# Kernel optimization log

Hardware: AMD Instinct MI355X
Metric: run time of the kernel (lower is better)

Reference implementation:

```python
import jax, jax.numpy as jnp
import numpy as np

B, LATENT = 8192, 1024
NR, NC = 12, 12                      # nb_rows, nb_cols
H0, W0 = NR + 2, NC + 2              # 14x14 after reshape
EPS = 1e-5
SLOPE = 0.01                         # LeakyReLU default


def setup_inputs() -> dict:
    key = jax.random.key(0)
    ks = jax.random.split(key, 9)
    s = 0.05
    return {
        "x": jax.random.normal(ks[0], (B, LATENT), jnp.float32),
        "fc_w": jax.random.normal(ks[1], (H0 * W0 * 36, LATENT), jnp.float32) * s,
        "fc_b": jax.random.normal(ks[2], (H0 * W0 * 36,), jnp.float32) * s,
        "conv_w": jax.random.normal(ks[3], (16, 36, 2, 2), jnp.float32) * s,
        "conv_b": jax.random.normal(ks[4], (16,), jnp.float32) * s,
        "gamma": jnp.ones((16,), jnp.float32),
        "beta": jnp.zeros((16,), jnp.float32),
        # locally-connected weights: (out_ch, in_ch, Hout, Wout, k*k)
        "lw1": jax.random.normal(ks[5], (6, 16, H0 - 1, W0 - 1, 4), jnp.float32) * s,
        "lw2": jax.random.normal(ks[6], (1, 6, H0 - 2, W0 - 2, 4), jnp.float32) * s,
    }


def _leaky(x):
    return jnp.where(x >= 0, x, SLOPE * x)


def _local_conv2(x, w):
    # x: (B,C,H,W); w: (O,C,Ho,Wo,4) with k=2, stride 1, no padding
    Ho, Wo = w.shape[2], w.shape[3]
    patches = jnp.stack(
        [x[:, :, dy:dy + Ho, dx:dx + Wo] for dy in (0, 1) for dx in (0, 1)],
        axis=-1)  # (B,C,Ho,Wo,4)
    return jnp.einsum('bchwk,ochwk->bohw', patches, w)


def reference(x, fc_w, fc_b, conv_w, conv_b, gamma, beta, lw1, lw2):
    # fc -> view(B, H0, W0, 36) -> permute to NCHW
    h = x @ fc_w.T + fc_b
    h = h.reshape(B, H0, W0, 36).transpose(0, 3, 1, 2)  # (B,36,14,14)
    # Conv2d k=2 padding='same' (torch pads bottom/right for even kernels)
    h = jax.lax.conv_general_dilated(
        h, conv_w, window_strides=(1, 1), padding=((0, 1), (0, 1)),
        dimension_numbers=('NCHW', 'OIHW', 'NCHW')) + conv_b[None, :, None, None]
    h = _leaky(h)
    # BatchNorm2d (training mode: batch stats, biased var)
    mu = h.mean(axis=(0, 2, 3), keepdims=True)
    var = h.var(axis=(0, 2, 3), keepdims=True)
    h = (h - mu) * jax.lax.rsqrt(var + EPS)
    h = h * gamma[None, :, None, None] + beta[None, :, None, None]
    # locally-connected stack: 14x14 -> 13x13 -> 12x12
    h = _leaky(_local_conv2(h, lw1))
    return _local_conv2(h, lw2)  # (B,1,12,12)
```

## Files before the change

kernel.cpp:

```cpp
#include <hip/hip_runtime.h>


#define SLOPE 0.01f

typedef __bf16 bf16x8 __attribute__((ext_vector_type(8)));
typedef float f32x4 __attribute__((ext_vector_type(4)));

typedef const __attribute__((address_space(1))) void* gas_ptr;
typedef __attribute__((address_space(3))) void* las_ptr;

__device__ __forceinline__ void load16_to_lds(const void* g, void* l) {
  __builtin_amdgcn_global_load_lds((gas_ptr)g, (las_ptr)l, 16, 0, 0);
}

__device__ __forceinline__ unsigned short f2bf(float f) {
  union { float f; unsigned int u; } v; v.f = f;
  unsigned int r = v.u + 0x7FFFu + ((v.u >> 16) & 1u);
  return (unsigned short)(r >> 16);
}
__device__ __forceinline__ float bfbits2f(unsigned int bits16) {
  union { unsigned int u; float f; } v; v.u = bits16 << 16;
  return v.f;
}
__device__ __forceinline__ float leaky(float v) { return v >= 0.f ? v : SLOPE * v; }

__global__ void k_cast_x(const float* __restrict__ x, unsigned short* __restrict__ xb,
                         float* __restrict__ stats) {
  if (blockIdx.x == 0 && threadIdx.x < 32) stats[threadIdx.x] = 0.f;
  int gid = blockIdx.x * 256 + threadIdx.x;
  const float4* x4 = (const float4*)x;
  float4 a = x4[gid * 2], b = x4[gid * 2 + 1];
  union { unsigned short s[8]; uint4 v; } o;
  o.s[0] = f2bf(a.x); o.s[1] = f2bf(a.y); o.s[2] = f2bf(a.z); o.s[3] = f2bf(a.w);
  o.s[4] = f2bf(b.x); o.s[5] = f2bf(b.y); o.s[6] = f2bf(b.z); o.s[7] = f2bf(b.w);
  ((uint4*)xb)[gid] = o.v;
}

__global__ void k_fold(const float* __restrict__ fc_w, const float* __restrict__ fc_b,
                       const float* __restrict__ conv_w, const float* __restrict__ conv_b,
                       unsigned short* __restrict__ Wc, float* __restrict__ bc) {
  __shared__ float cw[2304];
  int blk = blockIdx.x, og = blockIdx.y, t = threadIdx.x;
  if (blk == 196) {
    if (og != 0) return;
    uint4 z = make_uint4(0, 0, 0, 0);
    uint4* dst = (uint4*)(Wc + 3136 * 1024);
    for (int i = t; i < 8192; i += 256) dst[i] = z;
    for (int i = 3136 + t; i < 3200; i += 256) bc[i] = 0.f;
    return;
  }
  for (int i = t; i < 2304; i += 256) cw[i] = conv_w[i];
  __syncthreads();
  int i0 = blk / 14, j0 = blk - (blk / 14) * 14;
  float acc[4][4];
#pragma unroll
  for (int o = 0; o < 4; o++)
#pragma unroll
    for (int q = 0; q < 4; q++) acc[o][q] = 0.f;
  for (int c = 0; c < 36; c++) {
#pragma unroll
    for (int dy = 0; dy < 2; dy++) {
      int ii = i0 + dy; if (ii > 13) continue;
#pragma unroll
      for (int dx = 0; dx < 2; dx++) {
        int jj = j0 + dx; if (jj > 13) continue;
        int row = (ii * 14 + jj) * 36 + c;
        float4 f = *(const float4*)(fc_w + row * 1024 + t * 4);
        int kk = dy * 2 + dx;
#pragma unroll
        for (int oo = 0; oo < 4; oo++) {
          int o = og * 4 + oo;
          float w = cw[(o * 36 + c) * 4 + kk];
          acc[oo][0] += w * f.x; acc[oo][1] += w * f.y;
          acc[oo][2] += w * f.z; acc[oo][3] += w * f.w;
        }
      }
    }
  }
#pragma unroll
  for (int oo = 0; oo < 4; oo++) {
    int o = og * 4 + oo;
    int n = o * 196 + i0 * 14 + j0;
    union { unsigned short s[4]; uint2 v; } u;
    u.s[0] = f2bf(acc[oo][0]); u.s[1] = f2bf(acc[oo][1]);
    u.s[2] = f2bf(acc[oo][2]); u.s[3] = f2bf(acc[oo][3]);
    *(uint2*)(Wc + n * 1024 + t * 4) = u.v;
  }
  if (og == 0 && t < 16) {
    int o = t;
    float b = conv_b[o];
    for (int c = 0; c < 36; c++)
      for (int dy = 0; dy < 2; dy++) {
        int ii = i0 + dy; if (ii > 13) continue;
        for (int dx = 0; dx < 2; dx++) {
          int jj = j0 + dx; if (jj > 13) continue;
          b += cw[(o * 36 + c) * 4 + dy * 2 + dx] * fc_b[(ii * 14 + jj) * 36 + c];
        }
      }
    bc[o * 196 + i0 * 14 + j0] = b;
  }
}

__global__ __launch_bounds__(256, 4) void k_gemm(const unsigned short* __restrict__ Xb,
                                                 const unsigned short* __restrict__ Wcb,
                                                 const float* __restrict__ bc,
                                                 unsigned short* __restrict__ h2,
                                                 float* __restrict__ stats) {
  __shared__ __align__(16) char lds[32768];
  __shared__ float red[4][4];
  const int t = threadIdx.x;
  const int w = t >> 6, lane = t & 63;
  const int quad = lane >> 4, l15 = lane & 15;
  const int m0 = blockIdx.y * 128, n0 = blockIdx.x * 128;
  const int mrow = t & 127, tko = t >> 7;
  const unsigned short* ga = Xb + (m0 + mrow) * 1024 + tko * 8;
  const unsigned short* gb = Wcb + (n0 + mrow) * 1024 + tko * 8;
  const int wbase = w * 1024;
  const int wm0 = (w >> 1) * 64, wn0 = (w & 1) * 64;

  f32x4 acc[4][4];
#pragma unroll
  for (int a = 0; a < 4; a++)
#pragma unroll
    for (int b = 0; b < 4; b++) acc[a][b] = (f32x4){0.f, 0.f, 0.f, 0.f};

  auto stage = [&](int buf, int kb) {
    char* sA = lds + buf * 16384;
    char* sB = sA + 8192;
    load16_to_lds(ga + kb,      sA + wbase);
    load16_to_lds(ga + kb + 16, sA + 4096 + wbase);
    load16_to_lds(gb + kb,      sB + wbase);
    load16_to_lds(gb + kb + 16, sB + 4096 + wbase);
  };
  auto compute = [&](int buf) {
    char* lA = lds + buf * 16384;
    char* lB = lA + 8192;
    bf16x8 af[4], bfr[4];
#pragma unroll
    for (int mb = 0; mb < 4; mb++)
      af[mb] = *(const bf16x8*)(lA + quad * 2048 + (wm0 + mb * 16 + l15) * 16);
#pragma unroll
    for (int nb = 0; nb < 4; nb++)
      bfr[nb] = *(const bf16x8*)(lB + quad * 2048 + (wn0 + nb * 16 + l15) * 16);
#pragma unroll
    for (int mb = 0; mb < 4; mb++)
#pragma unroll
      for (int nb = 0; nb < 4; nb++)
        acc[mb][nb] = __builtin_amdgcn_mfma_f32_16x16x32_bf16(af[mb], bfr[nb], acc[mb][nb], 0, 0, 0);
  };

  stage(0, 0);
  __syncthreads();
  int cur = 0;
  for (int kb = 0; kb < 992; kb += 32) {
    stage(cur ^ 1, kb + 32);
    compute(cur);
    __syncthreads();
    cur ^= 1;
  }
  compute(cur);

  const int cLo = n0 / 196;
  const int cHi = (n0 + 127) / 196;
  float ss0 = 0.f, ss1 = 0.f, sq0 = 0.f, sq1 = 0.f;
#pragma unroll
  for (int nb = 0; nb < 4; nb++) {
    int col = n0 + wn0 + nb * 16 + l15;
    float bias = bc[col];
    int ch = col / 196;
    bool hi = (ch != cLo);
    bool valid = col < 3136;
    float cs = 0.f, cq = 0.f;
#pragma unroll
    for (int mb = 0; mb < 4; mb++) {
#pragma unroll
      for (int r = 0; r < 4; r++) {
        int row = m0 + wm0 + mb * 16 + quad * 4 + r;
        float v = leaky(acc[mb][nb][r] + bias);
        h2[row * 3200 + col] = f2bf(v);
        cs += v; cq += v * v;
      }
    }
    if (valid) {
      if (hi) { ss1 += cs; sq1 += cq; } else { ss0 += cs; sq0 += cq; }
    }
  }
#pragma unroll
  for (int off = 1; off < 64; off <<= 1) {
    ss0 += __shfl_xor(ss0, off, 64);
    ss1 += __shfl_xor(ss1, off, 64);
    sq0 += __shfl_xor(sq0, off, 64);
    sq1 += __shfl_xor(sq1, off, 64);
  }
  if (lane == 0) { red[w][0] = ss0; red[w][1] = ss1; red[w][2] = sq0; red[w][3] = sq1; }
  __syncthreads();
  if (t == 0) {
    float a0 = red[0][0] + red[1][0] + red[2][0] + red[3][0];
    float a1 = red[0][1] + red[1][1] + red[2][1] + red[3][1];
    float b0 = red[0][2] + red[1][2] + red[2][2] + red[3][2];
    float b1 = red[0][3] + red[1][3] + red[2][3] + red[3][3];
    atomicAdd(&stats[cLo], a0);
    atomicAdd(&stats[16 + cLo], b0);
    if (cHi != cLo && cHi < 16) {
      atomicAdd(&stats[cHi], a1);
      atomicAdd(&stats[16 + cHi], b1);
    }
  }
}

__global__ __launch_bounds__(256) void k_tail(const unsigned short* __restrict__ h2,
                                              const float* __restrict__ stats,
                                              const float* __restrict__ gamma,
                                              const float* __restrict__ beta,
                                              const float* __restrict__ lw1,
                                              const float* __restrict__ lw2,
                                              float* __restrict__ out) {
  __shared__ unsigned short h3[4 * 3138];
  __shared__ float h4[4 * 1015];
  __shared__ float sc[16], sh[16];
  int b0 = blockIdx.x * 4, t = threadIdx.x;
  if (t < 16) {
    const float inv = 1.f / 1605632.f;
    float mean = stats[t] * inv;
    float var = stats[16 + t] * inv - mean * mean;
    float rstd = rsqrtf(var + 1e-5f);
    float s = gamma[t] * rstd;
    sc[t] = s; sh[t] = beta[t] - mean * s;
  }
  __syncthreads();
  for (int i = t; i < 6272; i += 256) {
    int bb = i / 1568, q = i - bb * 1568;
    int n = q * 2, o = n / 196;
    unsigned int u = *(const unsigned int*)(h2 + (b0 + bb) * 3200 + n);
    float v0 = bfbits2f(u & 0xffffu) * sc[o] + sh[o];
    float v1 = bfbits2f(u >> 16) * sc[o] + sh[o];
    unsigned int pk = (unsigned int)f2bf(v0) | ((unsigned int)f2bf(v1) << 16);
    *(unsigned int*)(h3 + bb * 3138 + n) = pk;
  }
  __syncthreads();
  for (int u = t; u < 312; u += 256) {
    int bb = u & 3, rest = u >> 2;
    int o = rest / 13, y = rest - o * 13;
    float acc[13];
#pragma unroll
    for (int x = 0; x < 13; x++) acc[x] = 0.f;
    const unsigned short* hb = h3 + bb * 3138;
    for (int c = 0; c < 16; c++) {
      float r0[14], r1[14];
      const unsigned int* p0 = (const unsigned int*)(hb + c * 196 + y * 14);
      const unsigned int* p1 = (const unsigned int*)(hb + c * 196 + (y + 1) * 14);
#pragma unroll
      for (int q = 0; q < 7; q++) {
        unsigned int v0 = p0[q], v1 = p1[q];
        r0[2 * q] = bfbits2f(v0 & 0xffffu); r0[2 * q + 1] = bfbits2f(v0 >> 16);
        r1[2 * q] = bfbits2f(v1 & 0xffffu); r1[2 * q + 1] = bfbits2f(v1 >> 16);
      }
      const float4* wp4 = (const float4*)(lw1 + (((o * 16 + c) * 13 + y) * 13) * 4);
#pragma unroll
      for (int x = 0; x < 13; x++) {
        float4 wv = wp4[x];
        acc[x] += r0[x] * wv.x + r0[x + 1] * wv.y +
                  r1[x] * wv.z + r1[x + 1] * wv.w;
      }
    }
#pragma unroll
    for (int x = 0; x < 13; x++)
      h4[bb * 1015 + (o * 13 + y) * 13 + x] = leaky(acc[x]);
  }
  __syncthreads();
  for (int oi = t; oi < 576; oi += 256) {
    int pos = oi >> 2, bb = oi & 3;
    int y = pos / 12, x = pos - y * 12;
    float a = 0.f;
    const float* hp = h4 + bb * 1015;
    const float4* w4 = (const float4*)lw2;
#pragma unroll
    for (int c = 0; c < 6; c++) {
      float4 wv = w4[(c * 12 + y) * 12 + x];
      int hb = c * 169 + y * 13 + x;
      a += hp[hb] * wv.x + hp[hb + 1] * wv.y +
           hp[hb + 13] * wv.z + hp[hb + 14] * wv.w;
    }
    out[(b0 + bb) * 144 + pos] = a;
  }
}

extern "C" void kernel_launch(void* const* d_in, const int* in_sizes, int n_in,
                              void* d_out, int out_size, void* d_ws, size_t ws_size,
                              hipStream_t stream) {
  const float* x      = (const float*)d_in[0];
  const float* fc_w   = (const float*)d_in[1];
  const float* fc_b   = (const float*)d_in[2];
  const float* conv_w = (const float*)d_in[3];
  const float* conv_b = (const float*)d_in[4];
  const float* gamma  = (const float*)d_in[5];
  const float* beta   = (const float*)d_in[6];
  const float* lw1    = (const float*)d_in[7];
  const float* lw2    = (const float*)d_in[8];

  char* ws = (char*)d_ws;
  unsigned short* Xb    = (unsigned short*)(ws);
  unsigned short* Wc    = (unsigned short*)(ws + 16777216);
  float*          bc    = (float*)(ws + 23330816);
  float*          stats = (float*)(ws + 23343616);
  unsigned short* h2    = (unsigned short*)(ws + 23343744);

  k_cast_x<<<4096, 256, 0, stream>>>(x, Xb, stats);
  k_fold<<<dim3(197, 4), 256, 0, stream>>>(fc_w, fc_b, conv_w, conv_b, Wc, bc);
  k_gemm<<<dim3(25, 64), 256, 0, stream>>>(Xb, Wc, bc, h2, stats);
  k_tail<<<2048, 256, 0, stream>>>(h2, stats, gamma, beta, lw1, lw2, (float*)d_out);
}
```

Baseline: 384.9 us.

## Use 256x256 GEMM tiles with 512 threads and XCD-aware block mapping

The fused fc+conv GEMM moves from 128x128 tiles with 256 threads to 256x256 tiles with 512 threads (8 waves, each 128x64). A 1-D grid is remapped so consecutive M blocks share an XCD for L2 reuse. The padded N is extended to 3328 with zeroed weights/bias. The double-buffered LDS pipeline is replaced by a single buffer with two barriers per k-step, which loses load/compute overlap. Stats atomics are computed per wave.

```diff
diff --git a/kernel.cpp b/kernel.cpp
--- a/kernel.cpp
+++ b/kernel.cpp
@@ -45,8 +45,8 @@
     if (og != 0) return;
     uint4 z = make_uint4(0, 0, 0, 0);
     uint4* dst = (uint4*)(Wc + 3136 * 1024);
-    for (int i = t; i < 8192; i += 256) dst[i] = z;
-    for (int i = 3136 + t; i < 3200; i += 256) bc[i] = 0.f;
+    for (int i = t; i < 24576; i += 256) dst[i] = z;
+    for (int i = 3136 + t; i < 3328; i += 256) bc[i] = 0.f;
     return;
   }
   for (int i = t; i < 2304; i += 256) cw[i] = conv_w[i];
@@ -101,87 +101,79 @@
   }
 }
 
-__global__ __launch_bounds__(256, 4) void k_gemm(const unsigned short* __restrict__ Xb,
+__global__ __launch_bounds__(512, 1) void k_gemm(const unsigned short* __restrict__ Xb,
                                                  const unsigned short* __restrict__ Wcb,
                                                  const float* __restrict__ bc,
                                                  unsigned short* __restrict__ h2,
                                                  float* __restrict__ stats) {
   __shared__ __align__(16) char lds[32768];
-  __shared__ float red[4][4];
+  __shared__ float red[8][4];
   const int t = threadIdx.x;
   const int w = t >> 6, lane = t & 63;
   const int quad = lane >> 4, l15 = lane & 15;
-  const int m0 = blockIdx.y * 128, n0 = blockIdx.x * 128;
-  const int mrow = t & 127, tko = t >> 7;
+  const int d = blockIdx.x;
+  const int xcd = d & 7, j = d >> 3;
+  const int mblk = xcd * 4 + (j & 3);
+  const int nblk = j >> 2;
+  const int m0 = mblk * 256, n0 = nblk * 256;
+  const int mrow = t & 255, tko = t >> 8;
   const unsigned short* ga = Xb + (m0 + mrow) * 1024 + tko * 8;
   const unsigned short* gb = Wcb + (n0 + mrow) * 1024 + tko * 8;
-  const int wbase = w * 1024;
-  const int wm0 = (w >> 1) * 64, wn0 = (w & 1) * 64;
-
-  f32x4 acc[4][4];
-#pragma unroll
-  for (int a = 0; a < 4; a++)
+  char* lA = lds;
+  char* lB = lds + 16384;
+  const int wm = w >> 2, wn = w & 3;
+  const int wm0 = wm * 128, wn0 = wn * 64;
+
+  f32x4 acc[8][4];
+#pragma unroll
+  for (int a = 0; a < 8; a++)
 #pragma unroll
     for (int b = 0; b < 4; b++) acc[a][b] = (f32x4){0.f, 0.f, 0.f, 0.f};
 
-  auto stage = [&](int buf, int kb) {
-    char* sA = lds + buf * 16384;
-    char* sB = sA + 8192;
-    load16_to_lds(ga + kb,      sA + wbase);
-    load16_to_lds(ga + kb + 16, sA + 4096 + wbase);
-    load16_to_lds(gb + kb,      sB + wbase);
-    load16_to_lds(gb + kb + 16, sB + 4096 + wbase);
-  };
-  auto compute = [&](int buf) {
-    char* lA = lds + buf * 16384;
-    char* lB = lA + 8192;
-    bf16x8 af[4], bfr[4];
-#pragma unroll
-    for (int mb = 0; mb < 4; mb++)
-      af[mb] = *(const bf16x8*)(lA + quad * 2048 + (wm0 + mb * 16 + l15) * 16);
+  for (int kb = 0; kb < 1024; kb += 32) {
+    __syncthreads();
+    load16_to_lds(ga + kb,      lA + t * 16);
+    load16_to_lds(ga + kb + 16, lA + 8192 + t * 16);
+    load16_to_lds(gb + kb,      lB + t * 16);
+    load16_to_lds(gb + kb + 16, lB + 8192 + t * 16);
+    __syncthreads();
+
+    bf16x8 af[8], bfr[4];
+#pragma unroll
+    for (int mb = 0; mb < 8; mb++)
+      af[mb] = *(const bf16x8*)(lA + quad * 4096 + (wm0 + mb * 16 + l15) * 16);
 #pragma unroll
     for (int nb = 0; nb < 4; nb++)
-      bfr[nb] = *(const bf16x8*)(lB + quad * 2048 + (wn0 + nb * 16 + l15) * 16);
-#pragma unroll
-    for (int mb = 0; mb < 4; mb++)
+      bfr[nb] = *(const bf16x8*)(lB + quad * 4096 + (wn0 + nb * 16 + l15) * 16);
+#pragma unroll
+    for (int mb = 0; mb < 8; mb++)
 #pragma unroll
       for (int nb = 0; nb < 4; nb++)
         acc[mb][nb] = __builtin_amdgcn_mfma_f32_16x16x32_bf16(af[mb], bfr[nb], acc[mb][nb], 0, 0, 0);
-  };
-
-  stage(0, 0);
-  __syncthreads();
-  int cur = 0;
-  for (int kb = 0; kb < 992; kb += 32) {
-    stage(cur ^ 1, kb + 32);
-    compute(cur);
-    __syncthreads();
-    cur ^= 1;
-  }
-  compute(cur);
-
-  const int cLo = n0 / 196;
-  const int cHi = (n0 + 127) / 196;
+  }
+
+  const int chLo = (n0 + wn0) / 196;
   float ss0 = 0.f, ss1 = 0.f, sq0 = 0.f, sq1 = 0.f;
 #pragma unroll
   for (int nb = 0; nb < 4; nb++) {
-    int col = n0 + wn0 + nb * 16 + l15;
+    int colb = n0 + wn0 + nb * 16;
+    int col = colb + l15;
     float bias = bc[col];
-    int ch = col / 196;
-    bool hi = (ch != cLo);
-    bool valid = col < 3136;
+    bool store_ok = colb < 3200;
+    bool cnt = colb < 3136;
+    bool hi = (col / 196) != chLo;
     float cs = 0.f, cq = 0.f;
 #pragma unroll
-    for (int mb = 0; mb < 4; mb++) {
+    for (int mb = 0; mb < 8; mb++) {
 #pragma unroll
       for (int r = 0; r < 4; r++) {
         int row = m0 + wm0 + mb * 16 + quad * 4 + r;
         float v = leaky(acc[mb][nb][r] + bias);
-        h2[row * 3200 + col] = f2bf(v);
+        if (store_ok) h2[row * 3200 + col] = f2bf(v);
         cs += v; cq += v * v;
       }
     }
-    if (valid) {
+    if (cnt) {
       if (hi) { ss1 += cs; sq1 += cq; } else { ss0 += cs; sq0 += cq; }
     }
   }
@@ -195,15 +187,17 @@
   if (lane == 0) { red[w][0] = ss0; red[w][1] = ss1; red[w][2] = sq0; red[w][3] = sq1; }
   __syncthreads();
   if (t == 0) {
-    float a0 = red[0][0] + red[1][0] + red[2][0] + red[3][0];
-    float a1 = red[0][1] + red[1][1] + red[2][1] + red[3][1];
-    float b0 = red[0][2] + red[1][2] + red[2][2] + red[3][2];
-    float b1 = red[0][3] + red[1][3] + red[2][3] + red[3][3];
-    atomicAdd(&stats[cLo], a0);
-    atomicAdd(&stats[16 + cLo], b0);
-    if (cHi != cLo && cHi < 16) {
-      atomicAdd(&stats[cHi], a1);
-      atomicAdd(&stats[16 + cHi], b1);
+#pragma unroll
+    for (int w2 = 0; w2 < 8; w2++) {
+      int cl = (n0 + (w2 & 3) * 64) / 196;
+      if (cl < 16) {
+        atomicAdd(&stats[cl], red[w2][0]);
+        atomicAdd(&stats[16 + cl], red[w2][2]);
+      }
+      if (cl + 1 < 16) {
+        atomicAdd(&stats[cl + 1], red[w2][1]);
+        atomicAdd(&stats[16 + cl + 1], red[w2][3]);
+      }
     }
   }
 }
@@ -301,12 +295,12 @@
   char* ws = (char*)d_ws;
   unsigned short* Xb    = (unsigned short*)(ws);
   unsigned short* Wc    = (unsigned short*)(ws + 16777216);
-  float*          bc    = (float*)(ws + 23330816);
-  float*          stats = (float*)(ws + 23343616);
-  unsigned short* h2    = (unsigned short*)(ws + 23343744);
+  float*          bc    = (float*)(ws + 23592960);
+  float*          stats = (float*)(ws + 23606272);
+  unsigned short* h2    = (unsigned short*)(ws + 23606400);
 
   k_cast_x<<<4096, 256, 0, stream>>>(x, Xb, stats);
   k_fold<<<dim3(197, 4), 256, 0, stream>>>(fc_w, fc_b, conv_w, conv_b, Wc, bc);
-  k_gemm<<<dim3(25, 64), 256, 0, stream>>>(Xb, Wc, bc, h2, stats);
+  k_gemm<<<416, 512, 0, stream>>>(Xb, Wc, bc, h2, stats);
   k_tail<<<2048, 256, 0, stream>>>(h2, stats, gamma, beta, lw1, lw2, (float*)d_out);
 }
```

Result: slower. 431.9 us (+12.2%).

## Single-buffer GEMM LDS and remap blocks for XCD-local L2 reuse

Applied to the files above, without the earlier changes.

Replaces the double-buffered LDS pipeline in the GEMM with a single 16KB buffer, loaded and consumed between two barriers per k-step. It also flattens the grid to 1D and remaps block ids so that each XCD handles a contiguous group of 8 M-tiles across all N-tiles, which is meant to improve L2 reuse of the X rows. The smaller LDS footprint may allow more resident blocks per CU. The cost is that global-to-LDS loads no longer overlap the MFMA work, leaving latency hiding to occupancy alone.

```diff
diff --git a/kernel.cpp b/kernel.cpp
--- a/kernel.cpp
+++ b/kernel.cpp
@@ -106,15 +106,21 @@
                                                  const float* __restrict__ bc,
                                                  unsigned short* __restrict__ h2,
                                                  float* __restrict__ stats) {
-  __shared__ __align__(16) char lds[32768];
+  __shared__ __align__(16) char lds[16384];
   __shared__ float red[4][4];
   const int t = threadIdx.x;
   const int w = t >> 6, lane = t & 63;
   const int quad = lane >> 4, l15 = lane & 15;
-  const int m0 = blockIdx.y * 128, n0 = blockIdx.x * 128;
+  const int bid = blockIdx.x;
+  const int xcd = bid & 7, j = bid >> 3;
+  const int mblk = xcd * 8 + (j & 7);
+  const int nblk = j >> 3;
+  const int m0 = mblk * 128, n0 = nblk * 128;
   const int mrow = t & 127, tko = t >> 7;
   const unsigned short* ga = Xb + (m0 + mrow) * 1024 + tko * 8;
   const unsigned short* gb = Wcb + (n0 + mrow) * 1024 + tko * 8;
+  char* lA = lds;
+  char* lB = lds + 8192;
   const int wbase = w * 1024;
   const int wm0 = (w >> 1) * 64, wn0 = (w & 1) * 64;
 
@@ -124,17 +130,14 @@
 #pragma unroll
     for (int b = 0; b < 4; b++) acc[a][b] = (f32x4){0.f, 0.f, 0.f, 0.f};
 
-  auto stage = [&](int buf, int kb) {
-    char* sA = lds + buf * 16384;
-    char* sB = sA + 8192;
-    load16_to_lds(ga + kb,      sA + wbase);
-    load16_to_lds(ga + kb + 16, sA + 4096 + wbase);
-    load16_to_lds(gb + kb,      sB + wbase);
-    load16_to_lds(gb + kb + 16, sB + 4096 + wbase);
-  };
-  auto compute = [&](int buf) {
-    char* lA = lds + buf * 16384;
-    char* lB = lA + 8192;
+  for (int kb = 0; kb < 1024; kb += 32) {
+    __syncthreads();
+    load16_to_lds(ga + kb,      lA + wbase);
+    load16_to_lds(ga + kb + 16, lA + 4096 + wbase);
+    load16_to_lds(gb + kb,      lB + wbase);
+    load16_to_lds(gb + kb + 16, lB + 4096 + wbase);
+    __syncthreads();
+
     bf16x8 af[4], bfr[4];
 #pragma unroll
     for (int mb = 0; mb < 4; mb++)
@@ -147,18 +150,7 @@
 #pragma unroll
       for (int nb = 0; nb < 4; nb++)
         acc[mb][nb] = __builtin_amdgcn_mfma_f32_16x16x32_bf16(af[mb], bfr[nb], acc[mb][nb], 0, 0, 0);
-  };
-
-  stage(0, 0);
-  __syncthreads();
-  int cur = 0;
-  for (int kb = 0; kb < 992; kb += 32) {
-    stage(cur ^ 1, kb + 32);
-    compute(cur);
-    __syncthreads();
-    cur ^= 1;
-  }
-  compute(cur);
+  }
 
   const int cLo = n0 / 196;
   const int cHi = (n0 + 127) / 196;
@@ -307,6 +299,6 @@
 
   k_cast_x<<<4096, 256, 0, stream>>>(x, Xb, stats);
   k_fold<<<dim3(197, 4), 256, 0, stream>>>(fc_w, fc_b, conv_w, conv_b, Wc, bc);
-  k_gemm<<<dim3(25, 64), 256, 0, stream>>>(Xb, Wc, bc, h2, stats);
+  k_gemm<<<1600, 256, 0, stream>>>(Xb, Wc, bc, h2, stats);
   k_tail<<<2048, 256, 0, stream>>>(h2, stats, gamma, beta, lw1, lw2, (float*)d_out);
 }
```

Result: faster. 371.9 us (-3.4%).
